# Performance work log

Hardware: AMD Instinct MI355X
Metric: run time of the kernel (lower is better)

Reference implementation:

```python
import jax, jax.numpy as jnp
import numpy as np


def setup_inputs() -> dict:
    key = jax.random.key(0)
    ks = jax.random.split(key, 5)
    B, T, S, D = 4, 32, 320, 768
    return {
        "x": jax.random.normal(ks[0], (B, T, S, D), dtype=jnp.float32),
        "qkv_w": jax.random.normal(ks[1], (D, 3 * D), dtype=jnp.float32) * 0.02,
        "qkv_b": jax.random.normal(ks[2], (3 * D,), dtype=jnp.float32) * 0.02,
        "out_w": jax.random.normal(ks[3], (D, D), dtype=jnp.float32) * 0.02,
        "out_b": jax.random.normal(ks[4], (D,), dtype=jnp.float32) * 0.02,
        "n_latents": 64,
        "n_heads": 12,
    }


def reference(x, qkv_w, qkv_b, out_w, out_b, n_latents, n_heads):
    B, T, S, D = x.shape
    H = n_heads
    hd = D // H
    scale = 1.0 / jnp.sqrt(jnp.asarray(hd, dtype=x.dtype))

    # qkv projection: [B,T,S,3D]
    qkv = jnp.einsum('btsd,de->btse', x, qkv_w) + qkv_b
    q, k, v = jnp.split(qkv, 3, axis=-1)
    # [B,T,S,H,hd]
    q = q.reshape(B, T, S, H, hd)
    k = k.reshape(B, T, S, H, hd)
    v = v.reshape(B, T, S, H, hd)

    # block-sparse mask: latent queries (rows < n_latents) cannot attend to
    # patch keys (cols >= n_latents); everything else allowed
    rows = jnp.arange(S) < n_latents          # latent query rows
    cols = jnp.arange(S) >= n_latents         # patch key cols
    allow = ~(rows[:, None] & cols[None, :])  # [S,S] bool

    # attention scores [B,T,H,Sq,Sk]
    scores = jnp.einsum('btqhd,btkhd->bthqk', q, k) * scale
    scores = jnp.where(allow, scores, -jnp.inf)
    attn = jax.nn.softmax(scores, axis=-1)

    y = jnp.einsum('bthqk,btkhd->btqhd', attn, v).reshape(B, T, S, D)
    return jnp.einsum('btsd,de->btse', y, out_w) + out_b
```

## Files before the change

### kernel.cpp

```cpp
#include <hip/hip_runtime.h>

typedef __attribute__((ext_vector_type(8))) short bf16x8;
typedef __attribute__((ext_vector_type(4))) float f32x4;
typedef __attribute__((ext_vector_type(16))) float f32x16;
typedef __attribute__((address_space(1))) void gvoid_t;
typedef __attribute__((address_space(3))) void lvoid_t;

#define DEVI __device__ __forceinline__

DEVI unsigned short f2bf(float f) {
    unsigned int u = __builtin_bit_cast(unsigned int, f);
    u += 0x7fffu + ((u >> 16) & 1u);
    return (unsigned short)(u >> 16);
}

DEVI unsigned cvt_pk_bf16(float a, float b) {
    unsigned r;
    asm("v_cvt_pk_bf16_f32 %0, %1, %2" : "=v"(r) : "v"(a), "v"(b));
    return r;
}

__global__ void k_convert(const float* __restrict__ in, unsigned short* __restrict__ out, int n8) {
    int i = blockIdx.x * 256 + threadIdx.x;
    if (i >= n8) return;
    const float4* p = (const float4*)in + (size_t)i * 2;
    float4 a = p[0], b = p[1];
    uint4 o;
    o.x = f2bf(a.x) | ((unsigned)f2bf(a.y) << 16);
    o.y = f2bf(a.z) | ((unsigned)f2bf(a.w) << 16);
    o.z = f2bf(b.x) | ((unsigned)f2bf(b.y) << 16);
    o.w = f2bf(b.z) | ((unsigned)f2bf(b.w) << 16);
    *((uint4*)out + i) = o;
}

__global__ void k_transpose(const float* __restrict__ w, unsigned short* __restrict__ wt, int K, int N) {
    __shared__ float tile[32][33];
    int n0 = blockIdx.x * 32, k0 = blockIdx.y * 32;
    int tx = threadIdx.x, ty = threadIdx.y;
#pragma unroll
    for (int r = 0; r < 32; r += 8)
        tile[ty + r][tx] = w[(size_t)(k0 + ty + r) * N + n0 + tx];
    __syncthreads();
#pragma unroll
    for (int r = 0; r < 32; r += 8)
        wt[(size_t)(n0 + ty + r) * K + k0 + tx] = f2bf(tile[tx][ty + r]);
}

template <bool OUT_BF16>
__global__ __launch_bounds__(256, 2) void k_gemm(const unsigned short* __restrict__ A,
                                                 const unsigned short* __restrict__ Bt,
                                                 const float* __restrict__ bias,
                                                 void* __restrict__ out,
                                                 int M, int N, int K) {
    __shared__ unsigned short As[128 * 32];
    __shared__ unsigned short Bs[128 * 32];

    int tid = threadIdx.x;
    int nwg = gridDim.x, bid = blockIdx.x;
    int q = nwg >> 3, r = nwg & 7;
    int xcd = bid & 7, lid = bid >> 3;
    int swz = ((xcd < r) ? xcd * (q + 1) : r * (q + 1) + (xcd - r) * q) + lid;
    int ntn = N >> 7;
    int bm = swz / ntn, bn = swz % ntn;

    int lane = tid & 63, wid = tid >> 6;
    int wm = (wid & 1) << 6, wn = (wid >> 1) << 6;
    int lr = lane & 15, lg = lane >> 4;

    int srow = tid >> 2;
    int scol = (tid & 3) << 3;
    const unsigned short* ag = A + (size_t)(bm * 128 + srow) * K + scol;
    const unsigned short* bg = Bt + (size_t)(bn * 128 + srow) * K + scol;

    f32x4 acc[4][4];
#pragma unroll
    for (int i = 0; i < 4; ++i)
#pragma unroll
        for (int j = 0; j < 4; ++j) acc[i][j] = (f32x4){0.f, 0.f, 0.f, 0.f};

    for (int k0 = 0; k0 < K; k0 += 32) {
#pragma unroll
        for (int p = 0; p < 2; ++p) {
            __builtin_amdgcn_global_load_lds((gvoid_t*)(ag + (size_t)p * 64 * K + k0),
                                             (lvoid_t*)(As + p * 2048 + tid * 8), 16, 0, 0);
            __builtin_amdgcn_global_load_lds((gvoid_t*)(bg + (size_t)p * 64 * K + k0),
                                             (lvoid_t*)(Bs + p * 2048 + tid * 8), 16, 0, 0);
        }
        __syncthreads();
        bf16x8 af[4], bfr[4];
#pragma unroll
        for (int mf = 0; mf < 4; ++mf)
            af[mf] = *(const bf16x8*)&As[(wm + mf * 16 + lr) * 32 + lg * 8];
#pragma unroll
        for (int nf = 0; nf < 4; ++nf)
            bfr[nf] = *(const bf16x8*)&Bs[(wn + nf * 16 + lr) * 32 + lg * 8];
#pragma unroll
        for (int mf = 0; mf < 4; ++mf)
#pragma unroll
            for (int nf = 0; nf < 4; ++nf)
                acc[mf][nf] = __builtin_amdgcn_mfma_f32_16x16x32_bf16(af[mf], bfr[nf], acc[mf][nf], 0, 0, 0);
        __syncthreads();
    }

#pragma unroll
    for (int mf = 0; mf < 4; ++mf)
#pragma unroll
        for (int nf = 0; nf < 4; ++nf) {
            int col = bn * 128 + wn + nf * 16 + lr;
            float bv = bias[col];
#pragma unroll
            for (int i = 0; i < 4; ++i) {
                int row = bm * 128 + wm + mf * 16 + lg * 4 + i;
                float v = acc[mf][nf][i] + bv;
                if (OUT_BF16)
                    ((unsigned short*)out)[(size_t)row * N + col] = f2bf(v);
                else
                    ((float*)out)[(size_t)row * N + col] = v;
            }
        }
}

__global__ __launch_bounds__(640) void k_attn2(const unsigned short* __restrict__ qkv,
                                               unsigned short* __restrict__ y) {
    int bt = blockIdx.x / 12, h = blockIdx.x % 12;
    const unsigned short* Qg = qkv + (size_t)bt * 320 * 2304 + h * 64;
    const unsigned short* Kg = Qg + 768;
    const unsigned short* Vg = Qg + 1536;

    __shared__ unsigned short Vt[64 * 40];

    int tid = threadIdx.x, w = tid >> 6, l = tid & 63;
    int q = l & 31, hh = l >> 5;
    int q0 = w * 32;
    int ntile = (w < 2) ? 2 : 10;

    bf16x8 qf[4];
#pragma unroll
    for (int c = 0; c < 4; ++c)
        qf[c] = *(const bf16x8*)(Qg + (size_t)(q0 + q) * 2304 + c * 16 + hh * 8);

    f32x16 o0 = (f32x16)0.f, o1 = (f32x16)0.f;
    float m = -3e38f, lsum = 0.f;
    const float SC = 0.125f * 1.44269504089f;

    for (int t = 0; t < 10; ++t) {
        if (tid < 512) {
            int sk = tid >> 4;
            int sd = (tid & 15) * 4;
            union { uint2 u; unsigned short s[4]; } vv;
            vv.u = *(const uint2*)(Vg + (size_t)(t * 32 + sk) * 2304 + sd);
#pragma unroll
            for (int j = 0; j < 4; ++j) {
                int d = sd + j;
                Vt[d * 40 + (sk ^ (((d >> 3) & 3) << 3))] = vv.s[j];
            }
        }
        __syncthreads();

        if (t < ntile) {
            int s0 = t * 32;
            bf16x8 kf[4];
#pragma unroll
            for (int c = 0; c < 4; ++c)
                kf[c] = *(const bf16x8*)(Kg + (size_t)(s0 + q) * 2304 + c * 16 + hh * 8);

            f32x16 sacc = (f32x16)0.f;
#pragma unroll
            for (int c = 0; c < 4; ++c)
                sacc = __builtin_amdgcn_mfma_f32_32x32x16_bf16(kf[c], qf[c], sacc, 0, 0, 0);

            float p[16];
            float tm = -3e38f;
#pragma unroll
            for (int r = 0; r < 16; ++r) {
                p[r] = sacc[r] * SC;
                tm = fmaxf(tm, p[r]);
            }
            tm = fmaxf(tm, __shfl_xor(tm, 32));
            if (!__all(tm <= m + 8.f)) {
                float mn = fmaxf(m, tm);
                float al = __builtin_amdgcn_exp2f(m - mn);
                lsum *= al;
#pragma unroll
                for (int r = 0; r < 16; ++r) { o0[r] *= al; o1[r] *= al; }
                m = mn;
            }
#pragma unroll
            for (int r = 0; r < 16; ++r) {
                p[r] = __builtin_amdgcn_exp2f(p[r] - m);
                lsum += p[r];
            }

            unsigned a0 = cvt_pk_bf16(p[0], p[1]);
            unsigned a1 = cvt_pk_bf16(p[2], p[3]);
            unsigned b0 = cvt_pk_bf16(p[4], p[5]);
            unsigned b1 = cvt_pk_bf16(p[6], p[7]);
            asm("v_permlane32_swap_b32 %0, %1" : "+v"(a0), "+v"(b0));
            asm("v_permlane32_swap_b32 %0, %1" : "+v"(a1), "+v"(b1));
            unsigned c0 = cvt_pk_bf16(p[8], p[9]);
            unsigned c1 = cvt_pk_bf16(p[10], p[11]);
            unsigned d0 = cvt_pk_bf16(p[12], p[13]);
            unsigned d1 = cvt_pk_bf16(p[14], p[15]);
            asm("v_permlane32_swap_b32 %0, %1" : "+v"(c0), "+v"(d0));
            asm("v_permlane32_swap_b32 %0, %1" : "+v"(c1), "+v"(d1));
            union { unsigned u[4]; bf16x8 v; } pf0, pf1;
            pf0.u[0] = a0; pf0.u[1] = a1; pf0.u[2] = b0; pf0.u[3] = b1;
            pf1.u[0] = c0; pf1.u[1] = c1; pf1.u[2] = d0; pf1.u[3] = d1;

            {
                int d = q;
                int sw = (d >> 3) & 3;
                bf16x8 va0 = *(const bf16x8*)&Vt[d * 40 + ((0 + hh) ^ sw) * 8];
                bf16x8 va1 = *(const bf16x8*)&Vt[d * 40 + ((2 + hh) ^ sw) * 8];
                o0 = __builtin_amdgcn_mfma_f32_32x32x16_bf16(va0, pf0.v, o0, 0, 0, 0);
                o0 = __builtin_amdgcn_mfma_f32_32x32x16_bf16(va1, pf1.v, o0, 0, 0, 0);
            }
            {
                int d = 32 + q;
                int sw = (d >> 3) & 3;
                bf16x8 va0 = *(const bf16x8*)&Vt[d * 40 + ((0 + hh) ^ sw) * 8];
                bf16x8 va1 = *(const bf16x8*)&Vt[d * 40 + ((2 + hh) ^ sw) * 8];
                o1 = __builtin_amdgcn_mfma_f32_32x32x16_bf16(va0, pf0.v, o1, 0, 0, 0);
                o1 = __builtin_amdgcn_mfma_f32_32x32x16_bf16(va1, pf1.v, o1, 0, 0, 0);
            }
        }
        __syncthreads();
    }

    lsum += __shfl_xor(lsum, 32);
    float inv = 1.f / lsum;
    unsigned short* yp = y + (size_t)(bt * 320 + q0 + q) * 768 + h * 64;
#pragma unroll
    for (int r = 0; r < 16; r += 2) {
        int dr = (r & 3) + 8 * (r >> 2) + 4 * hh;
        *(unsigned*)(yp + dr) =
            (unsigned)f2bf(o0[r] * inv) | ((unsigned)f2bf(o0[r + 1] * inv) << 16);
        *(unsigned*)(yp + 32 + dr) =
            (unsigned)f2bf(o1[r] * inv) | ((unsigned)f2bf(o1[r + 1] * inv) << 16);
    }
}

extern "C" void kernel_launch(void* const* d_in, const int* in_sizes, int n_in,
                              void* d_out, int out_size, void* d_ws, size_t ws_size,
                              hipStream_t stream) {
    const float* x     = (const float*)d_in[0];
    const float* qkv_w = (const float*)d_in[1];
    const float* qkv_b = (const float*)d_in[2];
    const float* out_w = (const float*)d_in[3];
    const float* out_b = (const float*)d_in[4];

    const int M = 40960;
    unsigned short* xb  = (unsigned short*)d_ws;
    unsigned short* w1t = xb + (size_t)M * 768;
    unsigned short* w2t = w1t + (size_t)2304 * 768;
    unsigned short* qkv = w2t + (size_t)768 * 768;
    unsigned short* yb  = qkv + (size_t)M * 2304;

    k_convert<<<(M * 768 / 8 + 255) / 256, 256, 0, stream>>>(x, xb, M * 768 / 8);
    k_transpose<<<dim3(2304 / 32, 768 / 32), dim3(32, 8), 0, stream>>>(qkv_w, w1t, 768, 2304);
    k_transpose<<<dim3(768 / 32, 768 / 32), dim3(32, 8), 0, stream>>>(out_w, w2t, 768, 768);

    k_gemm<true><<<(M / 128) * (2304 / 128), 256, 0, stream>>>(xb, w1t, qkv_b, (void*)qkv, M, 2304, 768);
    k_attn2<<<128 * 12, 640, 0, stream>>>(qkv, yb);
    k_gemm<false><<<(M / 128) * (768 / 128), 256, 0, stream>>>(yb, w2t, out_b, d_out, M, 768, 768);
}
```

Measured before the change: 468.0 us.

## Replace GEMM with 256x256 tiled, double-buffered, swizzled-LDS pipelined kernel

Replaces the simple 128x128 bf16 GEMM, which synchronised on every 32-wide K step, with a 256x256-tile, 512-thread kernel. It uses 64-wide K tiles, double-buffered LDS with XOR-swizzled columns to avoid bank conflicts, and staged global-to-LDS prefetch interleaved with four MFMA phases per iteration under setprio. The aim is to hide memory latency and raise data reuse for both projections. The cost is 128 KB of LDS per block and heavy register use, which limits occupancy, plus more complex barrier and waitcnt scheduling that could be fragile.

```diff
diff --git a/kernel.cpp b/kernel.cpp
--- a/kernel.cpp
+++ b/kernel.cpp
@@ -18,6 +18,10 @@
     unsigned r;
     asm("v_cvt_pk_bf16_f32 %0, %1, %2" : "=v"(r) : "v"(a), "v"(b));
     return r;
+}
+
+DEVI f32x4 mfma16(bf16x8 a, bf16x8 b, f32x4 c) {
+    return __builtin_amdgcn_mfma_f32_16x16x32_bf16(a, b, c, 0, 0, 0);
 }
 
 __global__ void k_convert(const float* __restrict__ in, unsigned short* __restrict__ out, int n8) {
@@ -47,70 +51,159 @@
 }
 
 template <bool OUT_BF16>
-__global__ __launch_bounds__(256, 2) void k_gemm(const unsigned short* __restrict__ A,
-                                                 const unsigned short* __restrict__ Bt,
-                                                 const float* __restrict__ bias,
-                                                 void* __restrict__ out,
-                                                 int M, int N, int K) {
-    __shared__ unsigned short As[128 * 32];
-    __shared__ unsigned short Bs[128 * 32];
-
-    int tid = threadIdx.x;
-    int nwg = gridDim.x, bid = blockIdx.x;
-    int q = nwg >> 3, r = nwg & 7;
-    int xcd = bid & 7, lid = bid >> 3;
-    int swz = ((xcd < r) ? xcd * (q + 1) : r * (q + 1) + (xcd - r) * q) + lid;
-    int ntn = N >> 7;
-    int bm = swz / ntn, bn = swz % ntn;
-
-    int lane = tid & 63, wid = tid >> 6;
-    int wm = (wid & 1) << 6, wn = (wid >> 1) << 6;
-    int lr = lane & 15, lg = lane >> 4;
-
-    int srow = tid >> 2;
-    int scol = (tid & 3) << 3;
-    const unsigned short* ag = A + (size_t)(bm * 128 + srow) * K + scol;
-    const unsigned short* bg = Bt + (size_t)(bn * 128 + srow) * K + scol;
-
-    f32x4 acc[4][4];
-#pragma unroll
-    for (int i = 0; i < 4; ++i)
+__global__ __launch_bounds__(512, 2) void k_gemm256(const unsigned short* __restrict__ A,
+                                                    const unsigned short* __restrict__ Bt,
+                                                    const float* __restrict__ bias,
+                                                    void* __restrict__ out,
+                                                    int M, int N, int K) {
+    __shared__ unsigned short smem[65536];
+
+    const int tid = threadIdx.x;
+    const int nwg = gridDim.x, bid = blockIdx.x;
+    const int q8 = nwg >> 3, r8 = nwg & 7;
+    const int xcd = bid & 7, lid = bid >> 3;
+    const int swz = ((xcd < r8) ? xcd * (q8 + 1) : r8 * (q8 + 1) + (xcd - r8) * q8) + lid;
+    const int ntn = N >> 8;
+    const int bm = swz / ntn, bn = swz % ntn;
+
+    const int lane = tid & 63, wid = tid >> 6;
+    const int wr = wid >> 2, wc = wid & 3;
+    const int lr = lane & 15, lg = lane >> 4;
+    const int cswz = (lr & 7) << 3;
+    const int col0 = (lg * 8) ^ cswz;
+
+    const int NT = K >> 6;
+
+    const int srowl = tid >> 3;
+    const int scole = ((tid & 7) ^ (srowl & 7)) << 3;
+    const unsigned short* aSrc = A  + (size_t)(bm * 256 + srowl) * K + scole;
+    const unsigned short* bSrc = Bt + (size_t)(bn * 256 + srowl) * K + scole;
+
+#define STG(matOff, srcBase, qq, koff, bufw)                                              \
+    __builtin_amdgcn_global_load_lds((gvoid_t*)((srcBase) + (size_t)(qq) * 64 * K + (koff)), \
+        (lvoid_t*)(smem + (matOff) + (bufw) * 16384 + (qq) * 4096 + tid * 8), 16, 0, 0)
+
+    f32x4 acc[8][4];
+#pragma unroll
+    for (int i = 0; i < 8; ++i)
 #pragma unroll
         for (int j = 0; j < 4; ++j) acc[i][j] = (f32x4){0.f, 0.f, 0.f, 0.f};
 
-    for (int k0 = 0; k0 < K; k0 += 32) {
-#pragma unroll
-        for (int p = 0; p < 2; ++p) {
-            __builtin_amdgcn_global_load_lds((gvoid_t*)(ag + (size_t)p * 64 * K + k0),
-                                             (lvoid_t*)(As + p * 2048 + tid * 8), 16, 0, 0);
-            __builtin_amdgcn_global_load_lds((gvoid_t*)(bg + (size_t)p * 64 * K + k0),
-                                             (lvoid_t*)(Bs + p * 2048 + tid * 8), 16, 0, 0);
-        }
-        __syncthreads();
-        bf16x8 af[4], bfr[4];
-#pragma unroll
-        for (int mf = 0; mf < 4; ++mf)
-            af[mf] = *(const bf16x8*)&As[(wm + mf * 16 + lr) * 32 + lg * 8];
-#pragma unroll
-        for (int nf = 0; nf < 4; ++nf)
-            bfr[nf] = *(const bf16x8*)&Bs[(wn + nf * 16 + lr) * 32 + lg * 8];
-#pragma unroll
-        for (int mf = 0; mf < 4; ++mf)
-#pragma unroll
-            for (int nf = 0; nf < 4; ++nf)
-                acc[mf][nf] = __builtin_amdgcn_mfma_f32_16x16x32_bf16(af[mf], bfr[nf], acc[mf][nf], 0, 0, 0);
-        __syncthreads();
+    {
+        const int k1 = (NT > 1) ? 64 : 0;
+        STG(0, aSrc, 0, 0, 0); STG(0, aSrc, 1, 0, 0); STG(0, aSrc, 2, 0, 0); STG(0, aSrc, 3, 0, 0);
+        STG(32768, bSrc, 0, 0, 0); STG(32768, bSrc, 1, 0, 0); STG(32768, bSrc, 2, 0, 0); STG(32768, bSrc, 3, 0, 0);
+        STG(0, aSrc, 0, k1, 1); STG(0, aSrc, 2, k1, 1);
+        asm volatile("s_waitcnt vmcnt(2)" ::: "memory");
+        __builtin_amdgcn_s_barrier();
     }
 
-#pragma unroll
-    for (int mf = 0; mf < 4; ++mf)
+#pragma unroll 1
+    for (int t = 0; t < NT; ++t) {
+        const int bufR = t & 1, bufW = bufR ^ 1;
+        const int ko1 = (t + 1 < NT) ? (t + 1) * 64 : 0;
+        const int ko2 = (t + 2 < NT) ? (t + 2) * 64 : 0;
+        const unsigned short* abuf = smem + bufR * 16384;
+        const unsigned short* bbuf = smem + 32768 + bufR * 16384;
+        bf16x8 af[4][2], bfr[2][2];
+
+#pragma unroll
+        for (int mf = 0; mf < 4; ++mf)
+#pragma unroll
+            for (int kk = 0; kk < 2; ++kk)
+                af[mf][kk] = *(const bf16x8*)(abuf + (wr * 128 + mf * 16 + lr) * 64 + (col0 ^ (kk * 32)));
+#pragma unroll
+        for (int j = 0; j < 2; ++j)
+#pragma unroll
+            for (int kk = 0; kk < 2; ++kk)
+                bfr[j][kk] = *(const bf16x8*)(bbuf + (wc * 64 + j * 16 + lr) * 64 + (col0 ^ (kk * 32)));
+        STG(32768, bSrc, 0, ko1, bufW); STG(32768, bSrc, 1, ko1, bufW);
+        __builtin_amdgcn_s_barrier();
+        asm volatile("s_waitcnt lgkmcnt(0)" ::: "memory");
+        __builtin_amdgcn_sched_barrier(0);
+        __builtin_amdgcn_s_setprio(1);
+#pragma unroll
+        for (int mf = 0; mf < 4; ++mf)
+#pragma unroll
+            for (int j = 0; j < 2; ++j)
+#pragma unroll
+                for (int kk = 0; kk < 2; ++kk)
+                    acc[mf][j] = mfma16(af[mf][kk], bfr[j][kk], acc[mf][j]);
+        __builtin_amdgcn_s_setprio(0);
+        __builtin_amdgcn_s_barrier();
+
+#pragma unroll
+        for (int j = 0; j < 2; ++j)
+#pragma unroll
+            for (int kk = 0; kk < 2; ++kk)
+                bfr[j][kk] = *(const bf16x8*)(bbuf + (wc * 64 + (2 + j) * 16 + lr) * 64 + (col0 ^ (kk * 32)));
+        STG(32768, bSrc, 2, ko1, bufW); STG(32768, bSrc, 3, ko1, bufW);
+        __builtin_amdgcn_s_barrier();
+        asm volatile("s_waitcnt lgkmcnt(0)" ::: "memory");
+        __builtin_amdgcn_sched_barrier(0);
+        __builtin_amdgcn_s_setprio(1);
+#pragma unroll
+        for (int mf = 0; mf < 4; ++mf)
+#pragma unroll
+            for (int j = 0; j < 2; ++j)
+#pragma unroll
+                for (int kk = 0; kk < 2; ++kk)
+                    acc[mf][2 + j] = mfma16(af[mf][kk], bfr[j][kk], acc[mf][2 + j]);
+        __builtin_amdgcn_s_setprio(0);
+        __builtin_amdgcn_s_barrier();
+
+#pragma unroll
+        for (int mf = 0; mf < 4; ++mf)
+#pragma unroll
+            for (int kk = 0; kk < 2; ++kk)
+                af[mf][kk] = *(const bf16x8*)(abuf + (wr * 128 + 64 + mf * 16 + lr) * 64 + (col0 ^ (kk * 32)));
+        STG(0, aSrc, 1, ko1, bufW); STG(0, aSrc, 3, ko1, bufW);
+        __builtin_amdgcn_s_barrier();
+        asm volatile("s_waitcnt lgkmcnt(0)" ::: "memory");
+        __builtin_amdgcn_sched_barrier(0);
+        __builtin_amdgcn_s_setprio(1);
+#pragma unroll
+        for (int mf = 0; mf < 4; ++mf)
+#pragma unroll
+            for (int j = 0; j < 2; ++j)
+#pragma unroll
+                for (int kk = 0; kk < 2; ++kk)
+                    acc[4 + mf][2 + j] = mfma16(af[mf][kk], bfr[j][kk], acc[4 + mf][2 + j]);
+        __builtin_amdgcn_s_setprio(0);
+        __builtin_amdgcn_s_barrier();
+
+#pragma unroll
+        for (int j = 0; j < 2; ++j)
+#pragma unroll
+            for (int kk = 0; kk < 2; ++kk)
+                bfr[j][kk] = *(const bf16x8*)(bbuf + (wc * 64 + j * 16 + lr) * 64 + (col0 ^ (kk * 32)));
+        STG(0, aSrc, 0, ko2, bufR); STG(0, aSrc, 2, ko2, bufR);
+        __builtin_amdgcn_s_barrier();
+        asm volatile("s_waitcnt lgkmcnt(0)" ::: "memory");
+        __builtin_amdgcn_sched_barrier(0);
+        __builtin_amdgcn_s_setprio(1);
+#pragma unroll
+        for (int mf = 0; mf < 4; ++mf)
+#pragma unroll
+            for (int j = 0; j < 2; ++j)
+#pragma unroll
+                for (int kk = 0; kk < 2; ++kk)
+                    acc[4 + mf][j] = mfma16(af[mf][kk], bfr[j][kk], acc[4 + mf][j]);
+        __builtin_amdgcn_s_setprio(0);
+        asm volatile("s_waitcnt vmcnt(2)" ::: "memory");
+        __builtin_amdgcn_s_barrier();
+    }
+#undef STG
+
+#pragma unroll
+    for (int mf = 0; mf < 8; ++mf)
 #pragma unroll
         for (int nf = 0; nf < 4; ++nf) {
-            int col = bn * 128 + wn + nf * 16 + lr;
+            int col = bn * 256 + wc * 64 + nf * 16 + lr;
             float bv = bias[col];
 #pragma unroll
             for (int i = 0; i < 4; ++i) {
-                int row = bm * 128 + wm + mf * 16 + lg * 4 + i;
+                int row = bm * 256 + wr * 128 + mf * 16 + lg * 4 + i;
                 float v = acc[mf][nf][i] + bv;
                 if (OUT_BF16)
                     ((unsigned short*)out)[(size_t)row * N + col] = f2bf(v);
@@ -260,7 +353,7 @@
     k_transpose<<<dim3(2304 / 32, 768 / 32), dim3(32, 8), 0, stream>>>(qkv_w, w1t, 768, 2304);
     k_transpose<<<dim3(768 / 32, 768 / 32), dim3(32, 8), 0, stream>>>(out_w, w2t, 768, 768);
 
-    k_gemm<true><<<(M / 128) * (2304 / 128), 256, 0, stream>>>(xb, w1t, qkv_b, (void*)qkv, M, 2304, 768);
+    k_gemm256<true><<<(M / 256) * (2304 / 256), 512, 0, stream>>>(xb, w1t, qkv_b, (void*)qkv, M, 2304, 768);
     k_attn2<<<128 * 12, 640, 0, stream>>>(qkv, yb);
-    k_gemm<false><<<(M / 128) * (768 / 128), 256, 0, stream>>>(yb, w2t, out_b, d_out, M, 768, 768);
-}
+    k_gemm256<false><<<(M / 256) * (768 / 256), 512, 0, stream>>>(yb, w2t, out_b, d_out, M, 768, 768);
+}
```

Result: faster. 438.7 us (-6.3%).
